# Optimization experiments

Hardware: AMD Instinct MI355X
Metric: run time of the kernel (lower is better)

Reference implementation:

```python
import jax, jax.numpy as jnp
import numpy as np
import math

# ---- static configuration (mirrors Renderer defaults) ----
S = 129                                 # density cube side
L = math.ceil(S * math.sqrt(3))         # padded/rotation cube side = 224
C_ABS = 0.2                             # absorption coefficient c
LIGHTS = [
    {'dir': (2, 1, 1),    'rgb': (1.0, 69.0 / 255.0, 25.0 / 255.0)},
    {'dir': (-1, 0.5, 0), 'rgb': (227.0 / 255.0, 1.0, 66.0 / 255.0)},
]


def yp_from_light(l):
    ld = np.asarray(l, dtype=np.float64)
    ld = ld / np.sqrt(np.sum(ld ** 2))
    y = -math.asin(ld[0])
    if ld[2] < 0:
        y = -math.pi - y
    y = y * 180.0 / math.pi
    p = math.asin(ld[1]) * 180.0 / math.pi
    return y, p


def rot_matrix(yaw_deg, pitch_deg, order):
    # yaw about the y (height) axis, pitch about the x axis, roll = 0
    y = math.radians(yaw_deg)
    p = math.radians(pitch_deg)
    Ry = np.array([[math.cos(y), 0.0, math.sin(y)],
                   [0.0, 1.0, 0.0],
                   [-math.sin(y), 0.0, math.cos(y)]], dtype=np.float32)
    Rp = np.array([[1.0, 0.0, 0.0],
                   [0.0, math.cos(p), -math.sin(p)],
                   [0.0, math.sin(p), math.cos(p)]], dtype=np.float32)
    return Ry @ Rp if order == 'ypr' else Rp @ Ry

# base normalized sampling grid (align_corners=True convention), (x,y,z) order
_lin = np.linspace(-1.0, 1.0, L, dtype=np.float32)
_zz, _yy, _xx = np.meshgrid(_lin, _lin, _lin, indexing='ij')
BASE_XYZ = np.stack([_xx, _yy, _zz], axis=-1)   # [L,L,L,3]


def rotate_volume(vol, R):
    """Trilinear resampling of vol [B,C,D,H,W] under rotation R (zero padding)."""
    B, Ch, D, H, W = vol.shape
    src = jnp.einsum('dhwc,kc->dhwk', jnp.asarray(BASE_XYZ), jnp.asarray(R))
    xs = (src[..., 0] + 1.0) * 0.5 * (W - 1)
    ys = (src[..., 1] + 1.0) * 0.5 * (H - 1)
    zs = (src[..., 2] + 1.0) * 0.5 * (D - 1)
    x0 = jnp.floor(xs).astype(jnp.int32)
    y0 = jnp.floor(ys).astype(jnp.int32)
    z0 = jnp.floor(zs).astype(jnp.int32)
    wx = (xs - x0).astype(vol.dtype)
    wy = (ys - y0).astype(vol.dtype)
    wz = (zs - z0).astype(vol.dtype)
    flat = vol.reshape(B, Ch, D * H * W)

    def gather(zi, yi, xi):
        inb = ((zi >= 0) & (zi < D) & (yi >= 0) & (yi < H) & (xi >= 0) & (xi < W)).astype(vol.dtype)
        idx = ((jnp.clip(zi, 0, D - 1) * H + jnp.clip(yi, 0, H - 1)) * W
               + jnp.clip(xi, 0, W - 1)).reshape(-1)
        return jnp.take(flat, idx, axis=2).reshape(B, Ch, D, H, W) * inb

    out = (gather(z0,     y0,     x0)     * ((1 - wz) * (1 - wy) * (1 - wx))
         + gather(z0,     y0,     x0 + 1) * ((1 - wz) * (1 - wy) * wx)
         + gather(z0,     y0 + 1, x0)     * ((1 - wz) * wy * (1 - wx))
         + gather(z0,     y0 + 1, x0 + 1) * ((1 - wz) * wy * wx)
         + gather(z0 + 1, y0,     x0)     * (wz * (1 - wy) * (1 - wx))
         + gather(z0 + 1, y0,     x0 + 1) * (wz * (1 - wy) * wx)
         + gather(z0 + 1, y0 + 1, x0)     * (wz * wy * (1 - wx))
         + gather(z0 + 1, y0 + 1, x0 + 1) * (wz * wy * wx))
    return out


def _revcumsum(a):
    # torch.flip(cumsum(flip(a,[2]),2),[2]) : reverse cumulative sum along depth
    return jnp.flip(jnp.cumsum(jnp.flip(a, 2), axis=2), 2)


def setup_inputs() -> dict:
    key = jax.random.key(0)
    d = jax.random.uniform(key, (1, 1, S, S, S), dtype=jnp.float32)
    return {'d': d}


def reference(d):
    bs, _, Sd, _, _ = d.shape
    i = L // 2 - Sd // 2
    j = i + Sd
    light_array = jnp.zeros((bs, 3, Sd, Sd, Sd), dtype=d.dtype)
    for l in LIGHTS:
        y, p = yp_from_light(l['dir'])
        up = jnp.zeros((bs, 1, L, L, L), dtype=d.dtype).at[:, :, i:j, i:j, i:j].set(d)
        up = rotate_volume(up, rot_matrix(y, p, 'ypr'))
        up = jnp.exp(-C_ABS * _revcumsum(up))           # transmittance toward light
        up = rotate_volume(up, rot_matrix(-y, -p, 'rpy'))
        color = jnp.asarray(l['rgb'], dtype=d.dtype).reshape(1, 3, 1, 1, 1)
        light_array = light_array + up[:, :, i:j, i:j, i:j] * color
    t = jnp.exp(-C_ABS * _revcumsum(d))                  # view-ray transmittance
    out = C_ABS * jnp.sum(d * light_array * t, axis=2)   # background = 0
    return jnp.clip(out, 0.0, 1.0)
```

## Files before the change

kernel.cpp:

```cpp
#include <hip/hip_runtime.h>
#include <hip/hip_fp16.h>
#include <math.h>

#ifndef M_PI
#define M_PI 3.14159265358979323846
#endif

#define SS   129
#define LL   224
#define LL2  (LL*LL)
#define LL3  (LL*LL*LL)
#define SS2  (SS*SS)
#define SS3  (SS*SS*SS)
#define CABS 0.2f
#define PAD  48

#define BLO 45.5f
#define BHI 178.5f

#define NT1  28
#define NTZ16 14
#define ROTG  (2 * NTZ16 * 784)
#define ROTCH 392
#define NT3  17
#define NBZ16 9
#define BACKG (2 * NBZ16 * 289)
#define BACKCH 17
#define BACKG_P 5304
#define NTZ  28

#define NSEG 16
#define SEGZ 9
#define DSEGT (NSEG * SS2)
#define PREB1 ((DSEGT + 255) / 256)
#define PRERUNB 7
#define N4   (SS3 / 4)
#define CVT4B ((N4 + 1 + 255) / 256)
#define PREG (PREB1 + PRERUNB + CVT4B)
#define SUFG (392 + PREB1)
#define TEXPB (2 * NTZ * LL2 / 2 / 256)

#define RBX 21
#define RBY 16
#define RBZ 18
#define RBN (RBX*RBY*RBZ)
#define RSXZ (RBX*RBZ)

#define BBX 21
#define BBY 16
#define BBZ 19
#define BBN (BBX*BBY*BBZ)
#define BSXZ (BBX*BBZ)

struct Mat3 { float m[9]; };
struct F3   { float x, y, z; };

__device__ __forceinline__ F3 tile_center(const Mat3& M, int ox, int oy, int oz) {
    float cbx = fmaf((float)ox + 3.5f, 2.0f / 223.0f, -1.0f);
    float cby = fmaf((float)oy + 3.5f, 2.0f / 223.0f, -1.0f);
    float cbz = fmaf((float)oz + 3.5f, 2.0f / 223.0f, -1.0f);
    F3 qc;
    qc.x = fmaf(fmaf(M.m[0], cbx, fmaf(M.m[1], cby, M.m[2] * cbz)), 111.5f, 111.5f);
    qc.y = fmaf(fmaf(M.m[3], cbx, fmaf(M.m[4], cby, M.m[5] * cbz)), 111.5f, 111.5f);
    qc.z = fmaf(fmaf(M.m[6], cbx, fmaf(M.m[7], cby, M.m[8] * cbz)), 111.5f, 111.5f);
    return qc;
}

__device__ __forceinline__ F3 tile_center16(const Mat3& M, int ox, int oy, int oz) {
    float cbx = fmaf((float)ox + 3.5f, 2.0f / 223.0f, -1.0f);
    float cby = fmaf((float)oy + 3.5f, 2.0f / 223.0f, -1.0f);
    float cbz = fmaf((float)oz + 7.5f, 2.0f / 223.0f, -1.0f);
    F3 qc;
    qc.x = fmaf(fmaf(M.m[0], cbx, fmaf(M.m[1], cby, M.m[2] * cbz)), 111.5f, 111.5f);
    qc.y = fmaf(fmaf(M.m[3], cbx, fmaf(M.m[4], cby, M.m[5] * cbz)), 111.5f, 111.5f);
    qc.z = fmaf(fmaf(M.m[6], cbx, fmaf(M.m[7], cby, M.m[8] * cbz)), 111.5f, 111.5f);
    return qc;
}

__device__ __forceinline__ bool tile_accept(F3 qc, F3 H) {
    return !(qc.x + H.x < BLO || qc.x - H.x > BHI ||
             qc.y + H.y < BLO || qc.y - H.y > BHI ||
             qc.z + H.z < BLO || qc.z - H.z > BHI);
}

__device__ __forceinline__ void qmap(const Mat3& M, int x, int y, int z,
                                     float& qx, float& qy, float& qz) {
    float bx = fmaf((float)x, 2.0f / 223.0f, -1.0f);
    float by = fmaf((float)y, 2.0f / 223.0f, -1.0f);
    float bz = fmaf((float)z, 2.0f / 223.0f, -1.0f);
    qx = fmaf(fmaf(M.m[0], bx, fmaf(M.m[1], by, M.m[2] * bz)), 111.5f, 111.5f);
    qy = fmaf(fmaf(M.m[3], bx, fmaf(M.m[4], by, M.m[5] * bz)), 111.5f, 111.5f);
    qz = fmaf(fmaf(M.m[6], bx, fmaf(M.m[7], by, M.m[8] * bz)), 111.5f, 111.5f);
}

__device__ __forceinline__ float fetch_d(const float* __restrict__ d, int z, int y, int x) {
    unsigned zz = (unsigned)(z - PAD), yy = (unsigned)(y - PAD), xx = (unsigned)(x - PAD);
    return (zz < (unsigned)SS && yy < (unsigned)SS && xx < (unsigned)SS)
        ? d[((int)zz * SS + (int)yy) * SS + (int)xx] : 0.0f;
}

__device__ __forceinline__ float fetch_d16(const __half* __restrict__ d, int z, int y, int x) {
    unsigned zz = (unsigned)(z - PAD), yy = (unsigned)(y - PAD), xx = (unsigned)(x - PAD);
    return (zz < (unsigned)SS && yy < (unsigned)SS && xx < (unsigned)SS)
        ? __half2float(d[((int)zz * SS + (int)yy) * SS + (int)xx]) : 0.0f;
}

__device__ __forceinline__ float fetch_T(const float* __restrict__ T, int z, int y, int x) {
    unsigned zz = (unsigned)z, yy = (unsigned)y, xx = (unsigned)x;
    return (zz < (unsigned)LL && yy < (unsigned)LL && xx < (unsigned)LL)
        ? T[((int)zz * LL + (int)yy) * LL + (int)xx] : 0.0f;
}

__device__ __forceinline__ float tri_T(const float* __restrict__ T, float qz, float qy, float qx) {
    int x0 = (int)floorf(qx), y0 = (int)floorf(qy), z0 = (int)floorf(qz);
    float wx = qx - (float)x0, wy = qy - (float)y0, wz = qz - (float)z0;
    float c000 = fetch_T(T, z0, y0, x0),     c001 = fetch_T(T, z0, y0, x0 + 1);
    float c010 = fetch_T(T, z0, y0 + 1, x0), c011 = fetch_T(T, z0, y0 + 1, x0 + 1);
    float c100 = fetch_T(T, z0 + 1, y0, x0),     c101 = fetch_T(T, z0 + 1, y0, x0 + 1);
    float c110 = fetch_T(T, z0 + 1, y0 + 1, x0), c111 = fetch_T(T, z0 + 1, y0 + 1, x0 + 1);
    float a00 = c000 + wx * (c001 - c000), a01 = c010 + wx * (c011 - c010);
    float a10 = c100 + wx * (c101 - c100), a11 = c110 + wx * (c111 - c110);
    float b0 = a00 + wy * (a01 - a00), b1 = a10 + wy * (a11 - a10);
    return b0 + wz * (b1 - b0);
}

__device__ __forceinline__ float tri_d_g(const float* __restrict__ d, float qz, float qy, float qx) {
    int x0 = (int)floorf(qx), y0 = (int)floorf(qy), z0 = (int)floorf(qz);
    float wx = qx - (float)x0, wy = qy - (float)y0, wz = qz - (float)z0;
    float c000 = fetch_d(d, z0, y0, x0),     c001 = fetch_d(d, z0, y0, x0 + 1);
    float c010 = fetch_d(d, z0, y0 + 1, x0), c011 = fetch_d(d, z0, y0 + 1, x0 + 1);
    float c100 = fetch_d(d, z0 + 1, y0, x0),     c101 = fetch_d(d, z0 + 1, y0, x0 + 1);
    float c110 = fetch_d(d, z0 + 1, y0 + 1, x0), c111 = fetch_d(d, z0 + 1, y0 + 1, x0 + 1);
    float a00 = c000 + wx * (c001 - c000), a01 = c010 + wx * (c011 - c010);
    float a10 = c100 + wx * (c101 - c100), a11 = c110 + wx * (c111 - c110);
    float b0 = a00 + wy * (a01 - a00), b1 = a10 + wy * (a11 - a10);
    return b0 + wz * (b1 - b0);
}

__device__ __forceinline__ float tri_rot(const float* __restrict__ S,
                                         float qx, float qy, float qz,
                                         int lox, int loy, int loz) {
    int x0 = (int)floorf(qx), y0 = (int)floorf(qy), z0 = (int)floorf(qz);
    float wx = qx - (float)x0, wy = qy - (float)y0, wz = qz - (float)z0;
    int i = (y0 - loy) * 378 + (z0 - loz) * 21 + (x0 - lox);
    float c000 = S[i],        c001 = S[i + 1];
    float cz0  = S[i + 21],   cz1  = S[i + 22];
    float cy0  = S[i + 378],  cy1  = S[i + 379];
    float cw0  = S[i + 399],  cw1  = S[i + 400];
    float a00 = c000 + wx * (c001 - c000);
    float a01 = cy0  + wx * (cy1  - cy0);
    float a10 = cz0  + wx * (cz1  - cz0);
    float a11 = cw0  + wx * (cw1  - cw0);
    float b0  = a00 + wy * (a01 - a00);
    float b1  = a10 + wy * (a11 - a10);
    return b0 + wz * (b1 - b0);
}

__device__ __forceinline__ float tri_back(const float* __restrict__ S,
                                          float qx, float qy, float qz,
                                          int lox, int loy, int loz) {
    int x0 = (int)floorf(qx), y0 = (int)floorf(qy), z0 = (int)floorf(qz);
    float wx = qx - (float)x0, wy = qy - (float)y0, wz = qz - (float)z0;
    int i = (y0 - loy) * 399 + (z0 - loz) * 21 + (x0 - lox);
    float c000 = S[i],        c001 = S[i + 1];
    float cz0  = S[i + 21],   cz1  = S[i + 22];
    float cy0  = S[i + 399],  cy1  = S[i + 400];
    float cw0  = S[i + 420],  cw1  = S[i + 421];
    float a00 = c000 + wx * (c001 - c000);
    float a01 = cy0  + wx * (cy1  - cy0);
    float a10 = cz0  + wx * (cz1  - cz0);
    float a11 = cw0  + wx * (cw1  - cw0);
    float b0  = a00 + wy * (a01 - a00);
    float b1  = a10 + wy * (a11 - a10);
    return b0 + wz * (b1 - b0);
}

__global__ __launch_bounds__(256) void k_pre(const float* __restrict__ d,
        float* __restrict__ Dseg, float* __restrict__ A,
        unsigned short* __restrict__ Run, __half* __restrict__ d16,
        Mat3 M0, Mat3 M1, F3 H0, F3 H1) {
    int b = blockIdx.x;
    if (b < PREB1) {
        int t = b * 256 + threadIdx.x;
        if (t < 2 * SS2) A[t] = 0.0f;
        if (t >= DSEGT) return;
        int seg = t / SS2, col = t - seg * SS2;
        int zs = seg * SEGZ, ze = min(SS, zs + SEGZ);
        float run = 0.0f;
        for (int z = zs; z < ze; ++z) run += d[z * SS2 + col];
        Dseg[t] = run;
    } else if (b < PREB1 + PRERUNB) {
        int id = (b - PREB1) * 256 + threadIdx.x;
        if (id >= 2 * 784) return;
        int l = id / 784, r = id - l * 784;
        int ty = r / 28, tx = r - ty * 28;
        const Mat3 M = l ? M1 : M0;
        const F3  H  = l ? H1 : H0;
        int t0 = -1, t1 = -1;
        for (int tz = 0; tz < NT1; ++tz) {
            F3 qc = tile_center(M, tx * 8, ty * 8, tz * 8);
            if (tile_accept(qc, H)) { if (t0 < 0) t0 = tz; t1 = tz; }
        }
        Run[id] = (t0 < 0) ? 0xFFFFu : (unsigned short)(t0 | (t1 << 8));
    } else {
        int t4 = (b - PREB1 - PRERUNB) * 256 + threadIdx.x;
        if (t4 < N4) {
            float4 v = ((const float4*)d)[t4];
            __half2* o = (__half2*)(d16 + 4 * t4);
            o[0] = __floats2half2_rn(v.x, v.y);
            o[1] = __floats2half2_rn(v.z, v.w);
        } else if (t4 == N4) {
            d16[SS3 - 1] = __float2half(d[SS3 - 1]);
        }
    }
}

__global__ __launch_bounds__(512) void k_rot(const __half* __restrict__ d16,
        __half* __restrict__ T0, __half* __restrict__ T1,
        float* __restrict__ S0, float* __restrict__ S1,
        const unsigned short* __restrict__ Run,
        Mat3 M0, Mat3 M1, F3 H0, F3 H1) {
    int n = blockIdx.x;
    int x8 = n & 7, i8 = n >> 3;
    int c = i8 / ROTCH, off = i8 - c * ROTCH;
    int b = (c * 8 + x8) * ROTCH + off;

    int light = b / (NTZ16 * 784);
    int r = b - light * (NTZ16 * 784);
    int tz16 = r / 784;
    int r2 = r - tz16 * 784;
    int tty = r2 / 28, ttx = r2 - tty * 28;

    unsigned short rt = Run[light * 784 + tty * 28 + ttx];
    if (rt == 0xFFFFu) return;
    int t0 = rt & 0xFF, t1 = rt >> 8;
    if (2 * tz16 + 1 < t0 || 2 * tz16 > t1) return;

    const Mat3 M = light ? M1 : M0;
    const F3  H  = light ? H1 : H0;
    __half* __restrict__ T   = light ? T1 : T0;
    float* __restrict__ Ssum = light ? S1 : S0;

    int ox = ttx * 8, oy = tty * 8, oz = tz16 * 16;
    F3 qc = tile_center16(M, ox, oy, oz);

    int lox = (int)floorf(qc.x - H.x);
    int loy = (int)floorf(qc.y - H.y);
    int loz = (int)floorf(qc.z - H.z);

    __shared__ float S[RBN];
    __shared__ float Sc[1024];
    int tid = threadIdx.x;

    if (tid < RSXZ) {
        int ix = tid % RBX, iz = tid / RBX;
        bool interior = (lox >= PAD) & (lox <= PAD + SS - RBX) &
                        (loy >= PAD) & (loy <= PAD + SS - RBY) &
                        (loz >= PAD) & (loz <= PAD + SS - RBZ);
        if (interior) {
            const __half* g = d16 + ((size_t)(loz + iz - PAD) * SS + (loy - PAD)) * SS
                                  + (lox + ix - PAD);
            #pragma unroll
            for (int j = 0; j < RBY; ++j)
                S[tid + j * RSXZ] = __half2float(g[j * SS]);
        } else {
            #pragma unroll
            for (int j = 0; j < RBY; ++j)
                S[tid + j * RSXZ] = fetch_d16(d16, loz + iz, loy + j, lox + ix);
        }
    }
    __syncthreads();

    int lx = tid & 7, ly = (tid >> 3) & 7, lz = tid >> 6;
    int col = tid & 63;
    float fx = (float)lx - 3.5f, fy = (float)ly - 3.5f, fz = (float)lz - 7.5f;
    float qx = qc.x + fmaf(M.m[0], fx, fmaf(M.m[1], fy, M.m[2] * fz));
    float qy = qc.y + fmaf(M.m[3], fx, fmaf(M.m[4], fy, M.m[5] * fz));
    float qz = qc.z + fmaf(M.m[6], fx, fmaf(M.m[7], fy, M.m[8] * fz));
    float v0 = tri_rot(S, qx, qy, qz, lox, loy, loz);
    float qx2 = qx + 8.0f * M.m[2];
    float qy2 = qy + 8.0f * M.m[5];
    float qz2 = qz + 8.0f * M.m[8];
    float v1 = tri_rot(S, qx2, qy2, qz2, lox, loy, loz);

    Sc[lz * 64 + col] = v0;
    Sc[(lz + 8) * 64 + col] = v1;
    __syncthreads();
    if (tid < 128) {
        int zz = tid >> 3, ly2 = tid & 7;
        const float4* Sc4 = (const float4*)Sc;
        float4 f0 = Sc4[zz * 16 + ly2 * 2];
        float4 f1 = Sc4[zz * 16 + ly2 * 2 + 1];
        union { __half2 h[4]; float4 v; } u;
        u.h[0] = __floats2half2_rn(f0.x, f0.y);
        u.h[1] = __floats2half2_rn(f0.z, f0.w);
        u.h[2] = __floats2half2_rn(f1.x, f1.y);
        u.h[3] = __floats2half2_rn(f1.z, f1.w);
        *(float4*)&T[(size_t)(oz + zz) * LL2 + (oy + ly2) * LL + ox] = u.v;
    } else if (tid < 256) {
        int t2 = tid - 128;
        int cc = t2 & 63, h = t2 >> 6;
        float s = 0.0f;
        #pragma unroll
        for (int k = 0; k < 8; ++k) s += Sc[(h * 8 + k) * 64 + cc];
        int so = (oy + (cc >> 3)) * LL + (ox + (cc & 7));
        Ssum[(2 * tz16 + h) * LL2 + so] = s;
    }
}

__global__ __launch_bounds__(256) void k_sufw(float* __restrict__ S0,
        float* __restrict__ S1, const unsigned short* __restrict__ Run,
        const float* __restrict__ d, const float* __restrict__ Dseg,
        __half* __restrict__ W) {
    int b = blockIdx.x;
    if (b < 392) {
        int l = b / 196;
        int col = (b - l * 196) * 256 + threadIdx.x;
        float* __restrict__ Ssum = l ? S1 : S0;
        int x = col % LL, y = col / LL;
        unsigned short r = Run[l * 784 + (y >> 3) * 28 + (x >> 3)];
        if (r == 0xFFFFu) return;
        int t0 = r & 0xFF, t1 = r >> 8;
        float vbuf[NTZ];
        #pragma unroll
        for (int t = 0; t < NTZ; ++t)
            vbuf[t] = (t >= t0 && t <= t1) ? Ssum[t * LL2 + col] : 0.0f;
        float run = 0.0f;
        #pragma unroll
        for (int t = NTZ - 1; t >= 0; --t) {
            if (t >= t0 && t <= t1) Ssum[t * LL2 + col] = run;
            run += vbuf[t];
        }
    } else {
        int t = (b - 392) * 256 + threadIdx.x;
        if (t >= DSEGT) return;
        int seg = t / SS2, col = t - seg * SS2;
        int zs = seg * SEGZ, ze = min(SS, zs + SEGZ);
        float run = 0.0f;
        for (int s2 = seg + 1; s2 < NSEG; ++s2) run += Dseg[s2 * SS2 + col];
        for (int z = ze - 1; z >= zs; --z) {
            float dv = d[z * SS2 + col];
            run += dv;
            W[z * SS2 + col] = __float2half(dv * __expf(-CABS * run));
        }
    }
}

__global__ __launch_bounds__(256) void k_texp(__half* __restrict__ T0,
        __half* __restrict__ T1, const float* __restrict__ S0,
        const float* __restrict__ S1, const unsigned short* __restrict__ Run) {
    int id = blockIdx.x * 256 + threadIdx.x;
    int light = id / (NTZ * LL2 / 2);
    int r = id - light * (NTZ * LL2 / 2);
    int t = r / (LL2 / 2), cp = r - t * (LL2 / 2);
    int col = cp * 2;
    int y = col / LL, x = col - y * LL;
    const unsigned short* Rl = Run + light * 784 + (y >> 3) * 28;
    unsigned short rtA = Rl[x >> 3];
    unsigned short rtB = Rl[(x + 1) >> 3];
    bool aA = (rtA != 0xFFFFu) && t >= (rtA & 0xFF) && t <= (rtA >> 8);
    bool aB = (rtB != 0xFFFFu) && t >= (rtB & 0xFF) && t <= (rtB >> 8);
    if (!aA && !aB) return;
    const float* __restrict__ Ssum = light ? S1 : S0;
    __half* __restrict__ T = light ? T1 : T0;
    float offA = aA ? Ssum[t * LL2 + col]     : 0.0f;
    float offB = aB ? Ssum[t * LL2 + col + 1] : 0.0f;
    __half2* Tp = (__half2*)(T + (size_t)(8 * t) * LL2 + col);
    float2 v[8];
    #pragma unroll
    for (int k = 0; k < 8; ++k) v[k] = __half22float2(Tp[k * (LL2 / 2)]);
    float sA = 0.0f, sB = 0.0f;
    #pragma unroll
    for (int k = 7; k >= 0; --k) { sA += v[k].x; sB += v[k].y; v[k].x = sA; v[k].y = sB; }
    #pragma unroll
    for (int k = 0; k < 8; ++k) {
        float eA = aA ? __expf(-CABS * (v[k].x + offA)) : v[k].x;
        float eB = aB ? __expf(-CABS * (v[k].y + offB)) : v[k].y;
        Tp[k * (LL2 / 2)] = __floats2half2_rn(eA, eB);
    }
}

template<bool BINT>
__global__ __launch_bounds__(512) void k_back(const __half* __restrict__ T0,
        const __half* __restrict__ T1, const __half* __restrict__ W,
        float* __restrict__ A0, float* __restrict__ A1,
        Mat3 M0, Mat3 M1, F3 H0, F3 H1) {
    int n = blockIdx.x;
    int x8 = n & 7, i8 = n >> 3;
    int c = i8 / BACKCH, off = i8 - c * BACKCH;
    int lb = (c * 8 + x8) * BACKCH + off;
    if (lb >= BACKG) return;

    int light = lb / (NBZ16 * 289); lb -= light * (NBZ16 * 289);
    int tz16 = lb / 289;
    int r2 = lb - tz16 * 289;
    int tty = r2 / 17, ttx = r2 - tty * 17;

    const Mat3 M = light ? M1 : M0;
    const F3  H  = light ? H1 : H0;
    const __half* __restrict__ T = light ? T1 : T0;
    float* __restrict__ A = light ? A1 : A0;

    int ox = ttx * 8, oy = tty * 8, oz = tz16 * 16;
    F3 qc = tile_center16(M, ox + PAD, oy + PAD, oz + PAD);
    int lox = (int)floorf(qc.x - H.x);
    int loy = (int)floorf(qc.y - H.y);
    int loz = (int)floorf(qc.z - H.z);

    __shared__ float S[BBN];
    __shared__ float Sc[512];
    int tid = threadIdx.x;

    if (tid < BSXZ) {
        int ix = tid % BBX, iz = tid / BBX;
        if (BINT) {
            const __half* tb = T + ((size_t)(loz + iz) * LL + loy) * LL + (lox + ix);
            #pragma unroll
            for (int j = 0; j < BBY; ++j)
                S[tid + j * BSXZ] = __half2float(tb[j * LL]);
        } else {
            #pragma unroll
            for (int j = 0; j < BBY; ++j) {
                int gz = loz + iz, gy = loy + j, gx = lox + ix;
                bool inb = ((unsigned)gz < (unsigned)LL) & ((unsigned)gy < (unsigned)LL)
                         & ((unsigned)gx < (unsigned)LL);
                S[tid + j * BSXZ] = inb
                    ? __half2float(T[((size_t)gz * LL + gy) * LL + gx]) : 0.0f;
            }
        }
    }
    __syncthreads();

    int lx = tid & 7, ly = (tid >> 3) & 7, lz = tid >> 6;
    int col = tid & 63;
    int x = ox + lx, y = oy + ly;
    float v0 = 0.0f, v1 = 0.0f;
    if (x < SS && y < SS) {
        float fx = (float)lx - 3.5f, fy = (float)ly - 3.5f, fz = (float)lz - 7.5f;
        float qx = qc.x + fmaf(M.m[0], fx, fmaf(M.m[1], fy, M.m[2] * fz));
        float qy = qc.y + fmaf(M.m[3], fx, fmaf(M.m[4], fy, M.m[5] * fz));
        float qz = qc.z + fmaf(M.m[6], fx, fmaf(M.m[7], fy, M.m[8] * fz));
        int z0 = oz + lz, z1 = oz + 8 + lz;
        if (z0 < SS)
            v0 = tri_back(S, qx, qy, qz, lox, loy, loz)
               * __half2float(W[(z0 * SS + y) * SS + x]);
        if (z1 < SS) {
            float qx2 = qx + 8.0f * M.m[2];
            float qy2 = qy + 8.0f * M.m[5];
            float qz2 = qz + 8.0f * M.m[8];
            v1 = tri_back(S, qx2, qy2, qz2, lox, loy, loz)
               * __half2float(W[(z1 * SS + y) * SS + x]);
        }
    }
    Sc[lz * 64 + col] = v0 + v1;
    __syncthreads();
    if (tid < 64) {
        float s = 0.0f;
        #pragma unroll
        for (int k = 0; k < 8; ++k) s += Sc[k * 64 + tid];
        int xx = ox + (tid & 7), yy = oy + (tid >> 3);
        if (xx < SS && yy < SS) atomicAdd(&A[yy * SS + xx], s);
    }
}

__global__ __launch_bounds__(256) void k_combine(const float* __restrict__ A0,
        const float* __restrict__ A1, float* __restrict__ out, F3 c0, F3 c1) {
    int i = blockIdx.x * 256 + threadIdx.x;
    if (i >= 3 * SS2) return;
    int ch = i / SS2, col = i - ch * SS2;
    float r0 = (ch == 0) ? c0.x : ((ch == 1) ? c0.y : c0.z);
    float r1 = (ch == 0) ? c1.x : ((ch == 1) ? c1.y : c1.z);
    float o = CABS * (A0[col] * r0 + A1[col] * r1);
    out[i] = fminf(fmaxf(o, 0.0f), 1.0f);
}

__global__ __launch_bounds__(256) void k_rot_full(const float* __restrict__ d,
                                                  float* __restrict__ T, Mat3 R) {
    int i = blockIdx.x * 256 + threadIdx.x;
    if (i >= LL3) return;
    int x = i % LL; int r = i / LL; int y = r % LL; int z = r / LL;
    float qx, qy, qz; qmap(R, x, y, z, qx, qy, qz);
    T[i] = tri_d_g(d, qz, qy, qx);
}

__global__ __launch_bounds__(256) void k_scan_full(float* __restrict__ T) {
    int col = blockIdx.x * 256 + threadIdx.x;
    if (col >= LL2) return;
    float run = 0.0f;
    for (int z = LL - 1; z >= 0; --z) {
        int idx = z * LL2 + col;
        run += T[idx];
        T[idx] = __expf(-CABS * run);
    }
}

__global__ __launch_bounds__(64) void k_fused_back(const float* __restrict__ T,
        const float* __restrict__ d, float* __restrict__ LA, Mat3 RT,
        float cr, float cg, float cb, int first) {
    int col = blockIdx.x * 64 + threadIdx.x;
    if (col >= SS2) return;
    int y = col / SS, x = col % SS;
    float run = 0.0f, acc = 0.0f;
    for (int z = SS - 1; z >= 0; --z) {
        float qx, qy, qz; qmap(RT, x + PAD, y + PAD, z + PAD, qx, qy, qz);
        float u = tri_T(T, qz, qy, qx);
        float dv = d[z * SS2 + col];
        run += dv;
        acc = fmaf(dv * __expf(-CABS * run), u, acc);
    }
    if (first) {
        LA[0 * SS2 + col] = acc * cr;
        LA[1 * SS2 + col] = acc * cg;
        LA[2 * SS2 + col] = acc * cb;
    } else {
        LA[0 * SS2 + col] += acc * cr;
        LA[1 * SS2 + col] += acc * cg;
        LA[2 * SS2 + col] += acc * cb;
    }
}

__global__ __launch_bounds__(256) void k_clip(const float* __restrict__ LA,
                                              float* __restrict__ out) {
    int i = blockIdx.x * 256 + threadIdx.x;
    if (i < 3 * SS2) out[i] = fminf(fmaxf(CABS * LA[i], 0.0f), 1.0f);
}

static void light_mats(const double ld_in[3], Mat3& R, Mat3& RT) {
    double n = sqrt(ld_in[0]*ld_in[0] + ld_in[1]*ld_in[1] + ld_in[2]*ld_in[2]);
    double l0 = ld_in[0]/n, l1 = ld_in[1]/n, l2 = ld_in[2]/n;
    double yv = -asin(l0);
    if (l2 < 0) yv = -M_PI - yv;
    double yd = yv * 180.0 / M_PI, pd = asin(l1) * 180.0 / M_PI;
    double yr = yd * M_PI / 180.0, pr = pd * M_PI / 180.0;
    float cy = (float)cos(yr), sy = (float)sin(yr), cp = (float)cos(pr), sp = (float)sin(pr);
    float m[9] = { cy,  sy*sp,  sy*cp,
                   0.f, cp,    -sp,
                  -sy,  cy*sp,  cy*cp };
    for (int i = 0; i < 9; ++i) R.m[i] = m[i];
    RT.m[0] = m[0]; RT.m[1] = m[3]; RT.m[2] = m[6];
    RT.m[3] = m[1]; RT.m[4] = m[4]; RT.m[5] = m[7];
    RT.m[6] = m[2]; RT.m[7] = m[5]; RT.m[8] = m[8];
}

static F3 half_span8(const Mat3& M) {
    F3 h;
    h.x = 3.5f * (fabsf(M.m[0]) + fabsf(M.m[1]) + fabsf(M.m[2])) + 0.05f;
    h.y = 3.5f * (fabsf(M.m[3]) + fabsf(M.m[4]) + fabsf(M.m[5])) + 0.05f;
    h.z = 3.5f * (fabsf(M.m[6]) + fabsf(M.m[7]) + fabsf(M.m[8])) + 0.05f;
    return h;
}

static F3 half_span16(const Mat3& M) {
    F3 h;
    h.x = 3.5f * (fabsf(M.m[0]) + fabsf(M.m[1])) + 7.5f * fabsf(M.m[2]) + 0.1f;
    h.y = 3.5f * (fabsf(M.m[3]) + fabsf(M.m[4])) + 7.5f * fabsf(M.m[5]) + 0.1f;
    h.z = 3.5f * (fabsf(M.m[6]) + fabsf(M.m[7])) + 7.5f * fabsf(M.m[8]) + 0.1f;
    return h;
}

static void h_qc16(const Mat3& M, double ox, double oy, double oz, double q[3]) {
    double cb[3] = { (ox + 3.5) * 2.0 / 223.0 - 1.0,
                     (oy + 3.5) * 2.0 / 223.0 - 1.0,
                     (oz + 7.5) * 2.0 / 223.0 - 1.0 };
    for (int k = 0; k < 3; ++k)
        q[k] = ((double)M.m[3*k] * cb[0] + (double)M.m[3*k+1] * cb[1]
              + (double)M.m[3*k+2] * cb[2]) * 111.5 + 111.5;
}

extern "C" void kernel_launch(void* const* d_in, const int* in_sizes, int n_in,
                              void* d_out, int out_size, void* d_ws, size_t ws_size,
                              hipStream_t stream) {
    const float* d = (const float*)d_in[0];
    float* out = (float*)d_out;

    const double dirs[2][3] = { {2.0, 1.0, 1.0}, {-1.0, 0.5, 0.0} };
    F3 c0 = { 1.0f, 69.0f / 255.0f, 25.0f / 255.0f };
    F3 c1 = { 227.0f / 255.0f, 1.0f, 66.0f / 255.0f };
    Mat3 R[2], RT[2];
    light_mats(dirs[0], R[0], RT[0]);
    light_mats(dirs[1], R[1], RT[1]);
    F3 H8[2]  = { half_span8(R[0]),  half_span8(R[1])  };
    F3 H16[2] = { half_span16(R[0]), half_span16(R[1]) };
    F3 HB[2]  = { half_span16(RT[0]), half_span16(RT[1]) };

    bool bint = true;
    for (int l = 0; l < 2 && bint; ++l) {
        double H[3] = { HB[l].x, HB[l].y, HB[l].z };
        int dim[3] = { BBX, BBY, BBZ };
        for (int tz = 0; tz < NBZ16 && bint; ++tz)
            for (int ty = 0; ty < NT3 && bint; ++ty)
                for (int tx = 0; tx < NT3; ++tx) {
                    double q[3]; h_qc16(RT[l], tx * 8 + PAD, ty * 8 + PAD, tz * 16 + PAD, q);
                    for (int k = 0; k < 3; ++k) {
                        int lo = (int)floor(q[k] - H[k]);
                        if (lo < 1 || lo + dim[k] > LL - 1) { bint = false; break; }
                    }
                    if (!bint) break;
                }
    }

    const size_t f32n = (size_t)(2 * NTZ * LL2 + NSEG * SS2 + 2 * SS2);
    const size_t need_A = f32n * 4 + (size_t)(SS3 + 2 * LL3) * 2 + 2 * 784 * 2;
    const size_t need_C = (size_t)(LL3 + 3 * SS2) * 4;

    if (ws_size >= need_A) {
        float* S0   = (float*)d_ws;
        float* S1   = S0 + NTZ * LL2;
        float* Dseg = S1 + NTZ * LL2;
        float* A0   = Dseg + NSEG * SS2;
        float* A1   = A0 + SS2;
        __half* d16 = (__half*)(A1 + SS2);
        __half* W   = d16;
        __half* T0  = d16 + SS3;
        __half* T1  = T0 + LL3;
        unsigned short* Run = (unsigned short*)(T1 + LL3);

        k_pre  <<<PREG, 256, 0, stream>>>(d, Dseg, A0, Run, d16,
                                          R[0], R[1], H8[0], H8[1]);
        k_rot  <<<ROTG, 512, 0, stream>>>(d16, T0, T1, S0, S1, Run,
                                          R[0], R[1], H16[0], H16[1]);
        k_sufw <<<SUFG, 256, 0, stream>>>(S0, S1, Run, d, Dseg, W);
        k_texp <<<TEXPB, 256, 0, stream>>>(T0, T1, S0, S1, Run);
        if (bint)
            k_back<true><<<BACKG_P, 512, 0, stream>>>(T0, T1, W, A0, A1,
                                                      RT[0], RT[1], HB[0], HB[1]);
        else
            k_back<false><<<BACKG_P, 512, 0, stream>>>(T0, T1, W, A0, A1,
                                                       RT[0], RT[1], HB[0], HB[1]);
        k_combine<<<(3 * SS2 + 255) / 256, 256, 0, stream>>>(A0, A1, out, c0, c1);
    } else if (ws_size >= need_C) {
        float* T  = (float*)d_ws;
        float* LA = T + LL3;
        for (int l = 0; l < 2; ++l) {
            k_rot_full <<<(LL3 + 255) / 256, 256, 0, stream>>>(d, T, R[l]);
            k_scan_full<<<(LL2 + 255) / 256, 256, 0, stream>>>(T);
            k_fused_back<<<(SS2 + 63) / 64, 64, 0, stream>>>(T, d, LA, RT[l],
                l ? c1.x : c0.x, l ? c1.y : c0.y, l ? c1.z : c0.z, l == 0);
        }
        k_clip<<<(3 * SS2 + 255) / 256, 256, 0, stream>>>(LA, out);
    }
}
```

Baseline: 168.2 us.

## Fold pre-pass into rotation kernel and read fp32 density directly

Removes the separate k_pre launch by appending its segment-sum and run-table blocks as extra blocks of k_rot, and drops the fp16 copy of the density so the rotation gathers fp32 input directly. Rotation tiles now decide culling with an inline tile_accept test instead of reading the precomputed run table, since that table is produced concurrently. This saves one launch and one conversion pass at the cost of fp32 global loads with twice the bytes in the rotation gather.

```diff
diff --git a/kernel.cpp b/kernel.cpp
--- a/kernel.cpp
+++ b/kernel.cpp
@@ -32,11 +32,10 @@
 #define NSEG 16
 #define SEGZ 9
 #define DSEGT (NSEG * SS2)
+#define EXB1 ((DSEGT + 511) / 512)
+#define EXB2 4
+#define ROTG_E (ROTG + EXB1 + EXB2)
 #define PREB1 ((DSEGT + 255) / 256)
-#define PRERUNB 7
-#define N4   (SS3 / 4)
-#define CVT4B ((N4 + 1 + 255) / 256)
-#define PREG (PREB1 + PRERUNB + CVT4B)
 #define SUFG (392 + PREB1)
 #define TEXPB (2 * NTZ * LL2 / 2 / 256)
 
@@ -97,12 +96,6 @@
     unsigned zz = (unsigned)(z - PAD), yy = (unsigned)(y - PAD), xx = (unsigned)(x - PAD);
     return (zz < (unsigned)SS && yy < (unsigned)SS && xx < (unsigned)SS)
         ? d[((int)zz * SS + (int)yy) * SS + (int)xx] : 0.0f;
-}
-
-__device__ __forceinline__ float fetch_d16(const __half* __restrict__ d, int z, int y, int x) {
-    unsigned zz = (unsigned)(z - PAD), yy = (unsigned)(y - PAD), xx = (unsigned)(x - PAD);
-    return (zz < (unsigned)SS && yy < (unsigned)SS && xx < (unsigned)SS)
-        ? __half2float(d[((int)zz * SS + (int)yy) * SS + (int)xx]) : 0.0f;
 }
 
 __device__ __forceinline__ float fetch_T(const float* __restrict__ T, int z, int y, int x) {
@@ -175,52 +168,42 @@
     return b0 + wz * (b1 - b0);
 }
 
-__global__ __launch_bounds__(256) void k_pre(const float* __restrict__ d,
-        float* __restrict__ Dseg, float* __restrict__ A,
-        unsigned short* __restrict__ Run, __half* __restrict__ d16,
-        Mat3 M0, Mat3 M1, F3 H0, F3 H1) {
-    int b = blockIdx.x;
-    if (b < PREB1) {
-        int t = b * 256 + threadIdx.x;
-        if (t < 2 * SS2) A[t] = 0.0f;
-        if (t >= DSEGT) return;
-        int seg = t / SS2, col = t - seg * SS2;
-        int zs = seg * SEGZ, ze = min(SS, zs + SEGZ);
-        float run = 0.0f;
-        for (int z = zs; z < ze; ++z) run += d[z * SS2 + col];
-        Dseg[t] = run;
-    } else if (b < PREB1 + PRERUNB) {
-        int id = (b - PREB1) * 256 + threadIdx.x;
-        if (id >= 2 * 784) return;
-        int l = id / 784, r = id - l * 784;
-        int ty = r / 28, tx = r - ty * 28;
-        const Mat3 M = l ? M1 : M0;
-        const F3  H  = l ? H1 : H0;
-        int t0 = -1, t1 = -1;
-        for (int tz = 0; tz < NT1; ++tz) {
-            F3 qc = tile_center(M, tx * 8, ty * 8, tz * 8);
-            if (tile_accept(qc, H)) { if (t0 < 0) t0 = tz; t1 = tz; }
-        }
-        Run[id] = (t0 < 0) ? 0xFFFFu : (unsigned short)(t0 | (t1 << 8));
-    } else {
-        int t4 = (b - PREB1 - PRERUNB) * 256 + threadIdx.x;
-        if (t4 < N4) {
-            float4 v = ((const float4*)d)[t4];
-            __half2* o = (__half2*)(d16 + 4 * t4);
-            o[0] = __floats2half2_rn(v.x, v.y);
-            o[1] = __floats2half2_rn(v.z, v.w);
-        } else if (t4 == N4) {
-            d16[SS3 - 1] = __float2half(d[SS3 - 1]);
-        }
-    }
-}
-
-__global__ __launch_bounds__(512) void k_rot(const __half* __restrict__ d16,
+__global__ __launch_bounds__(512) void k_rot(const float* __restrict__ d,
         __half* __restrict__ T0, __half* __restrict__ T1,
         float* __restrict__ S0, float* __restrict__ S1,
-        const unsigned short* __restrict__ Run,
-        Mat3 M0, Mat3 M1, F3 H0, F3 H1) {
+        float* __restrict__ Dseg, float* __restrict__ A,
+        unsigned short* __restrict__ Run,
+        Mat3 M0, Mat3 M1, F3 H0, F3 H1, F3 G0, F3 G1) {
     int n = blockIdx.x;
+    int tid = threadIdx.x;
+    if (n >= ROTG) {
+        int e = n - ROTG;
+        if (e < EXB1) {
+            int t = e * 512 + tid;
+            if (t < 2 * SS2) A[t] = 0.0f;
+            if (t >= DSEGT) return;
+            int seg = t / SS2, col = t - seg * SS2;
+            int zs = seg * SEGZ, ze = min(SS, zs + SEGZ);
+            float run = 0.0f;
+            for (int z = zs; z < ze; ++z) run += d[z * SS2 + col];
+            Dseg[t] = run;
+        } else {
+            int id = (e - EXB1) * 512 + tid;
+            if (id >= 2 * 784) return;
+            int l = id / 784, r = id - l * 784;
+            int ty = r / 28, tx = r - ty * 28;
+            const Mat3 M = l ? M1 : M0;
+            const F3  G  = l ? G1 : G0;
+            int t0 = -1, t1 = -1;
+            for (int tz = 0; tz < NT1; ++tz) {
+                F3 qc = tile_center(M, tx * 8, ty * 8, tz * 8);
+                if (tile_accept(qc, G)) { if (t0 < 0) t0 = tz; t1 = tz; }
+            }
+            Run[id] = (t0 < 0) ? 0xFFFFu : (unsigned short)(t0 | (t1 << 8));
+        }
+        return;
+    }
+
     int x8 = n & 7, i8 = n >> 3;
     int c = i8 / ROTCH, off = i8 - c * ROTCH;
     int b = (c * 8 + x8) * ROTCH + off;
@@ -231,11 +214,6 @@
     int r2 = r - tz16 * 784;
     int tty = r2 / 28, ttx = r2 - tty * 28;
 
-    unsigned short rt = Run[light * 784 + tty * 28 + ttx];
-    if (rt == 0xFFFFu) return;
-    int t0 = rt & 0xFF, t1 = rt >> 8;
-    if (2 * tz16 + 1 < t0 || 2 * tz16 > t1) return;
-
     const Mat3 M = light ? M1 : M0;
     const F3  H  = light ? H1 : H0;
     __half* __restrict__ T   = light ? T1 : T0;
@@ -243,6 +221,7 @@
 
     int ox = ttx * 8, oy = tty * 8, oz = tz16 * 16;
     F3 qc = tile_center16(M, ox, oy, oz);
+    if (!tile_accept(qc, H)) return;
 
     int lox = (int)floorf(qc.x - H.x);
     int loy = (int)floorf(qc.y - H.y);
@@ -250,7 +229,6 @@
 
     __shared__ float S[RBN];
     __shared__ float Sc[1024];
-    int tid = threadIdx.x;
 
     if (tid < RSXZ) {
         int ix = tid % RBX, iz = tid / RBX;
@@ -258,15 +236,15 @@
                         (loy >= PAD) & (loy <= PAD + SS - RBY) &
                         (loz >= PAD) & (loz <= PAD + SS - RBZ);
         if (interior) {
-            const __half* g = d16 + ((size_t)(loz + iz - PAD) * SS + (loy - PAD)) * SS
-                                  + (lox + ix - PAD);
+            const float* g = d + ((size_t)(loz + iz - PAD) * SS + (loy - PAD)) * SS
+                               + (lox + ix - PAD);
             #pragma unroll
             for (int j = 0; j < RBY; ++j)
-                S[tid + j * RSXZ] = __half2float(g[j * SS]);
+                S[tid + j * RSXZ] = g[j * SS];
         } else {
             #pragma unroll
             for (int j = 0; j < RBY; ++j)
-                S[tid + j * RSXZ] = fetch_d16(d16, loz + iz, loy + j, lox + ix);
+                S[tid + j * RSXZ] = fetch_d(d, loz + iz, loy + j, lox + ix);
         }
     }
     __syncthreads();
@@ -609,16 +587,13 @@
         float* Dseg = S1 + NTZ * LL2;
         float* A0   = Dseg + NSEG * SS2;
         float* A1   = A0 + SS2;
-        __half* d16 = (__half*)(A1 + SS2);
-        __half* W   = d16;
-        __half* T0  = d16 + SS3;
+        __half* W   = (__half*)(A1 + SS2);
+        __half* T0  = W + SS3;
         __half* T1  = T0 + LL3;
         unsigned short* Run = (unsigned short*)(T1 + LL3);
 
-        k_pre  <<<PREG, 256, 0, stream>>>(d, Dseg, A0, Run, d16,
-                                          R[0], R[1], H8[0], H8[1]);
-        k_rot  <<<ROTG, 512, 0, stream>>>(d16, T0, T1, S0, S1, Run,
-                                          R[0], R[1], H16[0], H16[1]);
+        k_rot  <<<ROTG_E, 512, 0, stream>>>(d, T0, T1, S0, S1, Dseg, A0, Run,
+                                            R[0], R[1], H16[0], H16[1], H8[0], H8[1]);
         k_sufw <<<SUFG, 256, 0, stream>>>(S0, S1, Run, d, Dseg, W);
         k_texp <<<TEXPB, 256, 0, stream>>>(T0, T1, S0, S1, Run);
         if (bint)
```

Result: no change. 166.0 us (-1.3%).
